# Optimization experiments

Hardware: AMD Instinct MI355X
Metric: run time of the kernel (lower is better)

## Reference

```python
import math
import jax, jax.numpy as jnp
import numpy as np

N_HEAD = 16

def new_gelu(x):
    # 0.5*x*(1+tanh(sqrt(2/pi)*(x+0.044715*x^3)))
    c = math.sqrt(2.0 / math.pi)
    return 0.5 * x * (1.0 + jnp.tanh(c * (x + 0.044715 * x * x * x)))

def setup_inputs() -> dict:
    key = jax.random.key(0)
    ks = jax.random.split(key, 9)
    B, T, C = 2, 2048, 1024
    s = lambda k, shape, fan: jax.random.normal(k, shape, dtype=jnp.float32) * (1.0 / math.sqrt(fan))
    return {
        "x": jax.random.normal(ks[0], (B, T, C), dtype=jnp.float32),
        "Wqkv": s(ks[1], (C, 3 * C), C),
        "bqkv": jnp.zeros((3 * C,), dtype=jnp.float32),
        "Wo": s(ks[2], (C, C), C),
        "bo": jnp.zeros((C,), dtype=jnp.float32),
        "Wfc": s(ks[3], (C, 4 * C), C),
        "bfc": jnp.zeros((4 * C,), dtype=jnp.float32),
        "Wproj": s(ks[4], (4 * C, C), 4 * C),
        "bproj": jnp.zeros((C,), dtype=jnp.float32),
    }

def attention(x, Wqkv, bqkv, Wo, bo):
    B, T, C = x.shape
    hd = C // N_HEAD
    xp = x @ Wqkv + bqkv                     # [B,T,3C]
    q, k, v = xp[:, :, :C], xp[:, :, C:2 * C], xp[:, :, 2 * C:]
    # Faithful to source: direct reshape [B,T,C] -> [B,nh,T,hd] (no transpose)
    q = q.reshape(B, N_HEAD, T, hd)
    k = k.reshape(B, N_HEAD, T, hd)
    v = v.reshape(B, N_HEAD, T, hd)
    att = jnp.einsum('bhqd,bhkd->bhqk', q, k) * (1.0 / math.sqrt(hd))
    causal = jnp.tril(jnp.ones((T, T), dtype=bool))
    att = jnp.where(causal, att, -jnp.inf)
    att = jax.nn.softmax(att, axis=-1)
    y = jnp.einsum('bhqk,bhkd->bhqd', att, v)  # [B,nh,T,hd]
    y = jnp.transpose(y, (0, 2, 1, 3)).reshape(B, T, C)
    return y @ Wo + bo

def reference(x, Wqkv, bqkv, Wo, bo, Wfc, bfc, Wproj, bproj):
    # Block.forward with layernorm=False (default), dropout in eval mode
    x = x + attention(x, Wqkv, bqkv, Wo, bo)
    mlpx = new_gelu(x @ Wfc + bfc) @ Wproj + bproj
    return x + mlpx
```

## Files before the change

### kernel.cpp

```cpp
#include <hip/hip_runtime.h>


typedef __attribute__((ext_vector_type(8))) short  bf16x8;
typedef __attribute__((ext_vector_type(4))) float  f32x4;
typedef __attribute__((ext_vector_type(8))) unsigned short u16x8;

__device__ __forceinline__ unsigned short bfu(float f) {
    union { float f; unsigned int u; } c; c.f = f;
    unsigned int u = c.u;
    unsigned int r = (u + 0x7fffu + ((u >> 16) & 1u)) >> 16;
    return (unsigned short)r;
}

__device__ __forceinline__ void gload_lds16(const void* g, void* l) {
    __builtin_amdgcn_global_load_lds(
        (const __attribute__((address_space(1))) void*)g,
        (__attribute__((address_space(3))) void*)l, 16, 0, 0);
}

__global__ __launch_bounds__(256) void cvt_bf16(const float* __restrict__ in,
                                                unsigned short* __restrict__ out) {
    size_t i = (size_t)blockIdx.x * 256 + threadIdx.x;
    const float4* p = (const float4*)in;
    float4 a = p[2 * i], b = p[2 * i + 1];
    u16x8 v;
    v[0] = bfu(a.x); v[1] = bfu(a.y); v[2] = bfu(a.z); v[3] = bfu(a.w);
    v[4] = bfu(b.x); v[5] = bfu(b.y); v[6] = bfu(b.z); v[7] = bfu(b.w);
    *(u16x8*)(out + 8 * i) = v;
}

__global__ __launch_bounds__(256) void wtrans(const float* __restrict__ W,
                                              unsigned short* __restrict__ Wt,
                                              int K, int N) {
    __shared__ float tile[32][33];
    int n0 = blockIdx.x * 32, k0 = blockIdx.y * 32;
    int tx = threadIdx.x & 31, ty = threadIdx.x >> 5;
#pragma unroll
    for (int r = 0; r < 32; r += 8)
        tile[ty + r][tx] = W[(size_t)(k0 + ty + r) * N + n0 + tx];
    __syncthreads();
#pragma unroll
    for (int r = 0; r < 32; r += 8)
        Wt[(size_t)(n0 + ty + r) * K + k0 + tx] = bfu(tile[tx][ty + r]);
}

template <int EPI>
__global__ __launch_bounds__(256) void gemm_bf16(
    const unsigned short* __restrict__ A, const unsigned short* __restrict__ Bt,
    const float* __restrict__ bias, const float* __restrict__ res,
    unsigned short* __restrict__ outb, float* __restrict__ outf,
    int M, int N, int K) {
    __shared__ __align__(16) unsigned short As[128 * 32];
    __shared__ __align__(16) unsigned short Bs[128 * 32];
    const int t = threadIdx.x;
    const int l = t & 63, w = t >> 6;
    const int lr = l & 15, lg = l >> 4;
    const int brow = blockIdx.y * 128, bcol = blockIdx.x * 128;
    const int wr = (w >> 1) * 64, wc = (w & 1) * 64;

    f32x4 acc[4][4];
#pragma unroll
    for (int m = 0; m < 4; ++m)
#pragma unroll
        for (int n = 0; n < 4; ++n) acc[m][n] = (f32x4){0.f, 0.f, 0.f, 0.f};

    const int ar = t >> 2, ac = (t & 3) * 8;
    const size_t Abase = (size_t)(brow + ar) * K + ac;
    const size_t Bbase = (size_t)(bcol + ar) * K + ac;
    char* la = (char*)As + w * 1024;
    char* lb = (char*)Bs + w * 1024;

    for (int kt = 0; kt < K; kt += 32) {
        gload_lds16(A + Abase + kt, la);
        gload_lds16(A + Abase + (size_t)64 * K + kt, la + 4096);
        gload_lds16(Bt + Bbase + kt, lb);
        gload_lds16(Bt + Bbase + (size_t)64 * K + kt, lb + 4096);
        __syncthreads();

        bf16x8 af[4], bfr[4];
#pragma unroll
        for (int m = 0; m < 4; ++m)
            af[m] = *(const bf16x8*)(As + (wr + m * 16 + lr) * 32 + lg * 8);
#pragma unroll
        for (int n = 0; n < 4; ++n)
            bfr[n] = *(const bf16x8*)(Bs + (wc + n * 16 + lr) * 32 + lg * 8);
#pragma unroll
        for (int m = 0; m < 4; ++m)
#pragma unroll
            for (int n = 0; n < 4; ++n)
                acc[m][n] = __builtin_amdgcn_mfma_f32_16x16x32_bf16(
                    af[m], bfr[n], acc[m][n], 0, 0, 0);
        __syncthreads();
    }

    float bv[4];
#pragma unroll
    for (int n = 0; n < 4; ++n) bv[n] = bias[bcol + wc + n * 16 + lr];
#pragma unroll
    for (int m = 0; m < 4; ++m) {
#pragma unroll
        for (int r = 0; r < 4; ++r) {
            const int row = brow + wr + m * 16 + lg * 4 + r;
#pragma unroll
            for (int n = 0; n < 4; ++n) {
                const int col = bcol + wc + n * 16 + lr;
                const size_t idx = (size_t)row * N + col;
                float v = acc[m][n][r] + bv[n];
                if constexpr (EPI == 0) {
                    outb[idx] = bfu(v);
                } else if constexpr (EPI == 1) {
                    v += res[idx];
                    outf[idx] = v;
                    outb[idx] = bfu(v);
                } else if constexpr (EPI == 2) {
                    float a = 0.7978845608f * (v + 0.044715f * v * v * v);
                    float g = v / (1.0f + __expf(-2.0f * a));
                    outb[idx] = bfu(g);
                } else {
                    v += res[idx];
                    outf[idx] = v;
                }
            }
        }
    }
}

__global__ __launch_bounds__(128) void attn(const unsigned short* __restrict__ xp,
                                            unsigned short* __restrict__ y) {
    __shared__ __align__(16) unsigned short Vt[64 * 72];
    __shared__ __align__(16) unsigned short Pl[2][32 * 72];
    const int t = threadIdx.x;
    const int l = t & 63, w = t >> 6;
    const int lr = l & 15, lg = l >> 4;
    const int bh = blockIdx.x >> 5;
    const int u = blockIdx.x & 31;
    const int qt = (u & 1) ? (31 - (u >> 1)) : (u >> 1);
    const int b = bh >> 4, h = bh & 15;
    const size_t hb = ((size_t)b * 2048 + h * 128) * 3072;
    const size_t rowb = (size_t)b * 2048;
    const int q0 = qt * 64 + w * 32;

    bf16x8 qf[2][2];
#pragma unroll
    for (int mq = 0; mq < 2; ++mq)
#pragma unroll
        for (int kk = 0; kk < 2; ++kk)
            qf[mq][kk] = *(const bf16x8*)(xp + hb + (size_t)((q0 >> 4) + mq) * 3072 +
                                          lr * 64 + kk * 32 + lg * 8);

    f32x4 o[2][4];
    float mx[2][4], ls[2][4];
#pragma unroll
    for (int mq = 0; mq < 2; ++mq)
#pragma unroll
        for (int n = 0; n < 4; ++n) o[mq][n] = (f32x4){0.f, 0.f, 0.f, 0.f};
#pragma unroll
    for (int mq = 0; mq < 2; ++mq)
#pragma unroll
        for (int r = 0; r < 4; ++r) { mx[mq][r] = -1e30f; ls[mq][r] = 0.f; }

    const int qmaxw = q0 + 31;
    const int ntiles = qt + 1;
    const int m32 = t & 31;
    const int cc = t >> 5;
    const float SC = 0.18033688f;

    for (int j = 0; j < ntiles; ++j) {
        const int kv0 = j * 64;
        __syncthreads();
#pragma unroll
        for (int it = 0; it < 4; ++it) {
            const int c = cc + it * 4;
            unsigned int xv[4];
#pragma unroll
            for (int n = 0; n < 4; ++n)
                xv[n] = *(const unsigned int*)(xp + hb + 2048 +
                                               (size_t)((kv0 >> 4) + n) * 3072 +
                                               c * 64 + 2 * m32);
            unsigned int lo0 = (xv[0] & 0xffffu) | (xv[1] << 16);
            unsigned int lo1 = (xv[2] & 0xffffu) | (xv[3] << 16);
            unsigned int hi0 = (xv[0] >> 16) | (xv[1] & 0xffff0000u);
            unsigned int hi1 = (xv[2] >> 16) | (xv[3] & 0xffff0000u);
            *(uint2*)(Vt + (2 * m32) * 72 + c * 4) = make_uint2(lo0, lo1);
            *(uint2*)(Vt + (2 * m32 + 1) * 72 + c * 4) = make_uint2(hi0, hi1);
        }
        __syncthreads();

        {
            f32x4 s[2][4];
#pragma unroll
            for (int mq = 0; mq < 2; ++mq)
#pragma unroll
                for (int n = 0; n < 4; ++n) s[mq][n] = (f32x4){0.f, 0.f, 0.f, 0.f};
#pragma unroll
            for (int kk = 0; kk < 2; ++kk)
#pragma unroll
                for (int n = 0; n < 4; ++n) {
                    bf16x8 kf = *(const bf16x8*)(xp + hb + 1024 +
                                                 (size_t)((kv0 >> 4) + n) * 3072 +
                                                 lr * 64 + kk * 32 + lg * 8);
#pragma unroll
                    for (int mq = 0; mq < 2; ++mq)
                        s[mq][n] = __builtin_amdgcn_mfma_f32_16x16x32_bf16(
                            qf[mq][kk], kf, s[mq][n], 0, 0, 0);
                }
            const bool needMask = (kv0 + 63) > q0;
#pragma unroll
            for (int mq = 0; mq < 2; ++mq)
#pragma unroll
                for (int n = 0; n < 4; ++n) {
                    s[mq][n] = s[mq][n] * SC;
                    if (needMask) {
                        const int col = kv0 + n * 16 + lr;
#pragma unroll
                        for (int r = 0; r < 4; ++r) {
                            const int row = q0 + mq * 16 + lg * 4 + r;
                            if (col > row) s[mq][n][r] = -1e30f;
                        }
                    }
                }
            float rmx[2][4], corr[2][4], rsum[2][4];
#pragma unroll
            for (int mq = 0; mq < 2; ++mq)
#pragma unroll
                for (int r = 0; r < 4; ++r)
                    rmx[mq][r] = fmaxf(fmaxf(s[mq][0][r], s[mq][1][r]),
                                       fmaxf(s[mq][2][r], s[mq][3][r]));
#pragma unroll
            for (int d = 1; d < 16; d <<= 1)
#pragma unroll
                for (int mq = 0; mq < 2; ++mq)
#pragma unroll
                    for (int r = 0; r < 4; ++r)
                        rmx[mq][r] = fmaxf(rmx[mq][r], __shfl_xor(rmx[mq][r], d, 64));
#pragma unroll
            for (int mq = 0; mq < 2; ++mq)
#pragma unroll
                for (int r = 0; r < 4; ++r) {
                    float mn = fmaxf(mx[mq][r], rmx[mq][r]);
                    corr[mq][r] = exp2f(mx[mq][r] - mn);
                    mx[mq][r] = mn;
                }
#pragma unroll
            for (int mq = 0; mq < 2; ++mq)
#pragma unroll
                for (int n = 0; n < 4; ++n)
#pragma unroll
                    for (int r = 0; r < 4; ++r)
                        s[mq][n][r] = exp2f(s[mq][n][r] - mx[mq][r]);
#pragma unroll
            for (int mq = 0; mq < 2; ++mq)
#pragma unroll
                for (int r = 0; r < 4; ++r)
                    rsum[mq][r] = s[mq][0][r] + s[mq][1][r] + s[mq][2][r] + s[mq][3][r];
#pragma unroll
            for (int d = 1; d < 16; d <<= 1)
#pragma unroll
                for (int mq = 0; mq < 2; ++mq)
#pragma unroll
                    for (int r = 0; r < 4; ++r)
                        rsum[mq][r] += __shfl_xor(rsum[mq][r], d, 64);
#pragma unroll
            for (int mq = 0; mq < 2; ++mq)
#pragma unroll
                for (int r = 0; r < 4; ++r)
                    ls[mq][r] = ls[mq][r] * corr[mq][r] + rsum[mq][r];
#pragma unroll
            for (int mq = 0; mq < 2; ++mq)
#pragma unroll
                for (int nd = 0; nd < 4; ++nd)
#pragma unroll
                    for (int r = 0; r < 4; ++r) o[mq][nd][r] *= corr[mq][r];
#pragma unroll
            for (int mq = 0; mq < 2; ++mq)
#pragma unroll
                for (int r = 0; r < 4; ++r) {
                    const int row = mq * 16 + lg * 4 + r;
                    unsigned int u0 = (unsigned)bfu(s[mq][0][r]) |
                                      ((unsigned)bfu(s[mq][1][r]) << 16);
                    unsigned int u1 = (unsigned)bfu(s[mq][2][r]) |
                                      ((unsigned)bfu(s[mq][3][r]) << 16);
                    *(uint2*)(&Pl[w][row * 72 + lr * 4]) = make_uint2(u0, u1);
                }
            asm volatile("s_waitcnt lgkmcnt(0)" ::: "memory");
            __builtin_amdgcn_sched_barrier(0);
#pragma unroll
            for (int kk = 0; kk < 2; ++kk) {
                bf16x8 pa[2];
                pa[0] = *(const bf16x8*)(&Pl[w][(lr) * 72 + kk * 32 + lg * 8]);
                pa[1] = *(const bf16x8*)(&Pl[w][(16 + lr) * 72 + kk * 32 + lg * 8]);
#pragma unroll
                for (int nd = 0; nd < 4; ++nd) {
                    bf16x8 vb = *(const bf16x8*)(Vt + (nd * 16 + lr) * 72 + kk * 32 + lg * 8);
                    o[0][nd] = __builtin_amdgcn_mfma_f32_16x16x32_bf16(pa[0], vb, o[0][nd], 0, 0, 0);
                    o[1][nd] = __builtin_amdgcn_mfma_f32_16x16x32_bf16(pa[1], vb, o[1][nd], 0, 0, 0);
                }
            }
        }
    }
#pragma unroll
    for (int mq = 0; mq < 2; ++mq)
#pragma unroll
        for (int r = 0; r < 4; ++r) {
            const float inv = 1.0f / ls[mq][r];
            const size_t row = rowb + q0 + mq * 16 + lg * 4 + r;
#pragma unroll
            for (int nd = 0; nd < 4; ++nd)
                y[row * 1024 + h * 64 + nd * 16 + lr] = bfu(o[mq][nd][r] * inv);
        }
}

extern "C" void kernel_launch(void* const* d_in, const int* in_sizes, int n_in,
                              void* d_out, int out_size, void* d_ws, size_t ws_size,
                              hipStream_t stream) {
    const float* x     = (const float*)d_in[0];
    const float* Wqkv  = (const float*)d_in[1];
    const float* bqkv  = (const float*)d_in[2];
    const float* Wo    = (const float*)d_in[3];
    const float* bo    = (const float*)d_in[4];
    const float* Wfc   = (const float*)d_in[5];
    const float* bfc   = (const float*)d_in[6];
    const float* Wproj = (const float*)d_in[7];
    const float* bproj = (const float*)d_in[8];
    float* out = (float*)d_out;

    char* p = (char*)d_ws;
    unsigned short* xb     = (unsigned short*)(p);
    unsigned short* xpb    = (unsigned short*)(p + (8ull << 20));
    unsigned short* hbuf   = (unsigned short*)(p);
    unsigned short* ybuf   = (unsigned short*)(p + (32ull << 20));
    float*          x1     = (float*)(p + (40ull << 20));
    unsigned short* x1b    = (unsigned short*)(p + (56ull << 20));
    unsigned short* WqkvT  = (unsigned short*)(p + (64ull << 20));
    unsigned short* WoT    = (unsigned short*)(p + (70ull << 20));
    unsigned short* WfcT   = (unsigned short*)(p + (72ull << 20));
    unsigned short* WprojT = (unsigned short*)(p + (80ull << 20));

    cvt_bf16<<<dim3(2048), 256, 0, stream>>>(x, xb);
    wtrans<<<dim3(96, 32), 256, 0, stream>>>(Wqkv, WqkvT, 1024, 3072);
    wtrans<<<dim3(32, 32), 256, 0, stream>>>(Wo, WoT, 1024, 1024);
    wtrans<<<dim3(128, 32), 256, 0, stream>>>(Wfc, WfcT, 1024, 4096);
    wtrans<<<dim3(32, 128), 256, 0, stream>>>(Wproj, WprojT, 4096, 1024);

    gemm_bf16<0><<<dim3(24, 32), 256, 0, stream>>>(xb, WqkvT, bqkv, nullptr,
                                                   xpb, nullptr, 4096, 3072, 1024);
    attn<<<dim3(1024), 128, 0, stream>>>(xpb, ybuf);
    gemm_bf16<1><<<dim3(8, 32), 256, 0, stream>>>(ybuf, WoT, bo, x,
                                                  x1b, x1, 4096, 1024, 1024);
    gemm_bf16<2><<<dim3(32, 32), 256, 0, stream>>>(x1b, WfcT, bfc, nullptr,
                                                   hbuf, nullptr, 4096, 4096, 1024);
    gemm_bf16<3><<<dim3(8, 32), 256, 0, stream>>>(hbuf, WprojT, bproj, x1,
                                                  nullptr, out, 4096, 1024, 4096);
}
```

Baseline: 487.5 us.

## Split attention KV loop across four wave groups with LDS softmax merge

The attention kernel now runs 512 threads per block: four groups of two waves each take every fourth KV tile for the same 64-query tile. The groups' partial output, max and sum states are then combined through shared memory with a two-step log-sum-exp merge. Block order is also changed so the longest query tiles launch first instead of interleaving short and long tiles. This targets long serial KV loops on the late query tiles and poor load balance. In exchange it adds extra block-wide barriers, 72KB of LDS per block and merge overhead, and the 4-wide KV split leaves groups idle on short tiles.

Result: faster. 460.1 us (-5.6%).

```diff
diff --git a/kernel.cpp b/kernel.cpp
--- a/kernel.cpp
+++ b/kernel.cpp
@@ -125,27 +125,30 @@
     }
 }
 
-__global__ __launch_bounds__(128) void attn(const unsigned short* __restrict__ xp,
-                                            unsigned short* __restrict__ y) {
-    __shared__ __align__(16) unsigned short Vt[64 * 72];
-    __shared__ __align__(16) unsigned short Pl[2][32 * 72];
+__global__ __launch_bounds__(512, 4) void attn(const unsigned short* __restrict__ xp,
+                                               unsigned short* __restrict__ y) {
+    __shared__ __align__(16) char smem[73728];
     const int t = threadIdx.x;
     const int l = t & 63, w = t >> 6;
+    const int s = w & 1, g = w >> 1;
     const int lr = l & 15, lg = l >> 4;
-    const int bh = blockIdx.x >> 5;
-    const int u = blockIdx.x & 31;
-    const int qt = (u & 1) ? (31 - (u >> 1)) : (u >> 1);
+    const int qt = 31 - (blockIdx.x >> 5);
+    const int bh = blockIdx.x & 31;
     const int b = bh >> 4, h = bh & 15;
     const size_t hb = ((size_t)b * 2048 + h * 128) * 3072;
     const size_t rowb = (size_t)b * 2048;
-    const int q0 = qt * 64 + w * 32;
+    const int q0 = qt * 64;
+    const int qmin = q0 + s * 32;
+
+    unsigned short* Vtg = (unsigned short*)smem + g * (64 * 72);
+    unsigned short* Plw = (unsigned short*)(smem + 36864) + w * (32 * 72);
 
     bf16x8 qf[2][2];
 #pragma unroll
     for (int mq = 0; mq < 2; ++mq)
 #pragma unroll
         for (int kk = 0; kk < 2; ++kk)
-            qf[mq][kk] = *(const bf16x8*)(xp + hb + (size_t)((q0 >> 4) + mq) * 3072 +
+            qf[mq][kk] = *(const bf16x8*)(xp + hb + (size_t)((qmin >> 4) + mq) * 3072 +
                                           lr * 64 + kk * 32 + lg * 8);
 
     f32x4 o[2][4];
@@ -159,39 +162,44 @@
 #pragma unroll
         for (int r = 0; r < 4; ++r) { mx[mq][r] = -1e30f; ls[mq][r] = 0.f; }
 
-    const int qmaxw = q0 + 31;
     const int ntiles = qt + 1;
-    const int m32 = t & 31;
-    const int cc = t >> 5;
+    const int niter = (qt + 4) >> 2;
+    const int tg = s * 64 + l;
+    const int m32 = tg & 31;
+    const int cc = tg >> 5;
     const float SC = 0.18033688f;
 
-    for (int j = 0; j < ntiles; ++j) {
+    for (int jj = 0; jj < niter; ++jj) {
+        const int j = jj * 4 + g;
+        const bool active = (j < ntiles);
         const int kv0 = j * 64;
         __syncthreads();
-#pragma unroll
-        for (int it = 0; it < 4; ++it) {
-            const int c = cc + it * 4;
-            unsigned int xv[4];
-#pragma unroll
-            for (int n = 0; n < 4; ++n)
-                xv[n] = *(const unsigned int*)(xp + hb + 2048 +
-                                               (size_t)((kv0 >> 4) + n) * 3072 +
-                                               c * 64 + 2 * m32);
-            unsigned int lo0 = (xv[0] & 0xffffu) | (xv[1] << 16);
-            unsigned int lo1 = (xv[2] & 0xffffu) | (xv[3] << 16);
-            unsigned int hi0 = (xv[0] >> 16) | (xv[1] & 0xffff0000u);
-            unsigned int hi1 = (xv[2] >> 16) | (xv[3] & 0xffff0000u);
-            *(uint2*)(Vt + (2 * m32) * 72 + c * 4) = make_uint2(lo0, lo1);
-            *(uint2*)(Vt + (2 * m32 + 1) * 72 + c * 4) = make_uint2(hi0, hi1);
+        if (active) {
+#pragma unroll
+            for (int it = 0; it < 4; ++it) {
+                const int c = cc + it * 4;
+                unsigned int xv[4];
+#pragma unroll
+                for (int n = 0; n < 4; ++n)
+                    xv[n] = *(const unsigned int*)(xp + hb + 2048 +
+                                                   (size_t)((kv0 >> 4) + n) * 3072 +
+                                                   c * 64 + 2 * m32);
+                unsigned int lo0 = (xv[0] & 0xffffu) | (xv[1] << 16);
+                unsigned int lo1 = (xv[2] & 0xffffu) | (xv[3] << 16);
+                unsigned int hi0 = (xv[0] >> 16) | (xv[1] & 0xffff0000u);
+                unsigned int hi1 = (xv[2] >> 16) | (xv[3] & 0xffff0000u);
+                *(uint2*)(Vtg + (2 * m32) * 72 + c * 4) = make_uint2(lo0, lo1);
+                *(uint2*)(Vtg + (2 * m32 + 1) * 72 + c * 4) = make_uint2(hi0, hi1);
+            }
         }
         __syncthreads();
 
-        {
-            f32x4 s[2][4];
-#pragma unroll
-            for (int mq = 0; mq < 2; ++mq)
-#pragma unroll
-                for (int n = 0; n < 4; ++n) s[mq][n] = (f32x4){0.f, 0.f, 0.f, 0.f};
+        if (active) {
+            f32x4 sv[2][4];
+#pragma unroll
+            for (int mq = 0; mq < 2; ++mq)
+#pragma unroll
+                for (int n = 0; n < 4; ++n) sv[mq][n] = (f32x4){0.f, 0.f, 0.f, 0.f};
 #pragma unroll
             for (int kk = 0; kk < 2; ++kk)
 #pragma unroll
@@ -201,21 +209,21 @@
                                                  lr * 64 + kk * 32 + lg * 8);
 #pragma unroll
                     for (int mq = 0; mq < 2; ++mq)
-                        s[mq][n] = __builtin_amdgcn_mfma_f32_16x16x32_bf16(
-                            qf[mq][kk], kf, s[mq][n], 0, 0, 0);
-                }
-            const bool needMask = (kv0 + 63) > q0;
+                        sv[mq][n] = __builtin_amdgcn_mfma_f32_16x16x32_bf16(
+                            qf[mq][kk], kf, sv[mq][n], 0, 0, 0);
+                }
+            const bool needMask = (kv0 + 63) > qmin;
 #pragma unroll
             for (int mq = 0; mq < 2; ++mq)
 #pragma unroll
                 for (int n = 0; n < 4; ++n) {
-                    s[mq][n] = s[mq][n] * SC;
+                    sv[mq][n] = sv[mq][n] * SC;
                     if (needMask) {
                         const int col = kv0 + n * 16 + lr;
 #pragma unroll
                         for (int r = 0; r < 4; ++r) {
-                            const int row = q0 + mq * 16 + lg * 4 + r;
-                            if (col > row) s[mq][n][r] = -1e30f;
+                            const int row = qmin + mq * 16 + lg * 4 + r;
+                            if (col > row) sv[mq][n][r] = -1e30f;
                         }
                     }
                 }
@@ -224,8 +232,8 @@
             for (int mq = 0; mq < 2; ++mq)
 #pragma unroll
                 for (int r = 0; r < 4; ++r)
-                    rmx[mq][r] = fmaxf(fmaxf(s[mq][0][r], s[mq][1][r]),
-                                       fmaxf(s[mq][2][r], s[mq][3][r]));
+                    rmx[mq][r] = fmaxf(fmaxf(sv[mq][0][r], sv[mq][1][r]),
+                                       fmaxf(sv[mq][2][r], sv[mq][3][r]));
 #pragma unroll
             for (int d = 1; d < 16; d <<= 1)
 #pragma unroll
@@ -247,12 +255,12 @@
                 for (int n = 0; n < 4; ++n)
 #pragma unroll
                     for (int r = 0; r < 4; ++r)
-                        s[mq][n][r] = exp2f(s[mq][n][r] - mx[mq][r]);
+                        sv[mq][n][r] = exp2f(sv[mq][n][r] - mx[mq][r]);
 #pragma unroll
             for (int mq = 0; mq < 2; ++mq)
 #pragma unroll
                 for (int r = 0; r < 4; ++r)
-                    rsum[mq][r] = s[mq][0][r] + s[mq][1][r] + s[mq][2][r] + s[mq][3][r];
+                    rsum[mq][r] = sv[mq][0][r] + sv[mq][1][r] + sv[mq][2][r] + sv[mq][3][r];
 #pragma unroll
             for (int d = 1; d < 16; d <<= 1)
 #pragma unroll
@@ -276,38 +284,86 @@
 #pragma unroll
                 for (int r = 0; r < 4; ++r) {
                     const int row = mq * 16 + lg * 4 + r;
-                    unsigned int u0 = (unsigned)bfu(s[mq][0][r]) |
-                                      ((unsigned)bfu(s[mq][1][r]) << 16);
-                    unsigned int u1 = (unsigned)bfu(s[mq][2][r]) |
-                                      ((unsigned)bfu(s[mq][3][r]) << 16);
-                    *(uint2*)(&Pl[w][row * 72 + lr * 4]) = make_uint2(u0, u1);
+                    unsigned int u0 = (unsigned)bfu(sv[mq][0][r]) |
+                                      ((unsigned)bfu(sv[mq][1][r]) << 16);
+                    unsigned int u1 = (unsigned)bfu(sv[mq][2][r]) |
+                                      ((unsigned)bfu(sv[mq][3][r]) << 16);
+                    *(uint2*)(Plw + row * 72 + lr * 4) = make_uint2(u0, u1);
                 }
             asm volatile("s_waitcnt lgkmcnt(0)" ::: "memory");
             __builtin_amdgcn_sched_barrier(0);
 #pragma unroll
             for (int kk = 0; kk < 2; ++kk) {
                 bf16x8 pa[2];
-                pa[0] = *(const bf16x8*)(&Pl[w][(lr) * 72 + kk * 32 + lg * 8]);
-                pa[1] = *(const bf16x8*)(&Pl[w][(16 + lr) * 72 + kk * 32 + lg * 8]);
+                pa[0] = *(const bf16x8*)(Plw + (lr) * 72 + kk * 32 + lg * 8);
+                pa[1] = *(const bf16x8*)(Plw + (16 + lr) * 72 + kk * 32 + lg * 8);
 #pragma unroll
                 for (int nd = 0; nd < 4; ++nd) {
-                    bf16x8 vb = *(const bf16x8*)(Vt + (nd * 16 + lr) * 72 + kk * 32 + lg * 8);
+                    bf16x8 vb = *(const bf16x8*)(Vtg + (nd * 16 + lr) * 72 + kk * 32 + lg * 8);
                     o[0][nd] = __builtin_amdgcn_mfma_f32_16x16x32_bf16(pa[0], vb, o[0][nd], 0, 0, 0);
                     o[1][nd] = __builtin_amdgcn_mfma_f32_16x16x32_bf16(pa[1], vb, o[1][nd], 0, 0, 0);
                 }
             }
         }
     }
-#pragma unroll
-    for (int mq = 0; mq < 2; ++mq)
-#pragma unroll
-        for (int r = 0; r < 4; ++r) {
-            const float inv = 1.0f / ls[mq][r];
-            const size_t row = rowb + q0 + mq * 16 + lg * 4 + r;
+
+    float* buf = (float*)smem;
+    auto bufw = [&](int bi) {
+        float* q = buf + (size_t)(bi * 64 + l) * 52;
+#pragma unroll
+        for (int mq = 0; mq < 2; ++mq) {
 #pragma unroll
             for (int nd = 0; nd < 4; ++nd)
-                y[row * 1024 + h * 64 + nd * 16 + lr] = bfu(o[mq][nd][r] * inv);
+                *(f32x4*)(q + mq * 16 + nd * 4) = o[mq][nd];
+            f32x4 mv = {mx[mq][0], mx[mq][1], mx[mq][2], mx[mq][3]};
+            f32x4 lv = {ls[mq][0], ls[mq][1], ls[mq][2], ls[mq][3]};
+            *(f32x4*)(q + 32 + mq * 4) = mv;
+            *(f32x4*)(q + 40 + mq * 4) = lv;
         }
+    };
+    auto bufm = [&](int bi) {
+        const float* q = buf + (size_t)(bi * 64 + l) * 52;
+#pragma unroll
+        for (int mq = 0; mq < 2; ++mq) {
+            f32x4 mv = *(const f32x4*)(q + 32 + mq * 4);
+            f32x4 lv = *(const f32x4*)(q + 40 + mq * 4);
+            f32x4 ob[4];
+#pragma unroll
+            for (int nd = 0; nd < 4; ++nd)
+                ob[nd] = *(const f32x4*)(q + mq * 16 + nd * 4);
+#pragma unroll
+            for (int r = 0; r < 4; ++r) {
+                float mn = fmaxf(mx[mq][r], mv[r]);
+                float ca = exp2f(mx[mq][r] - mn);
+                float cb = exp2f(mv[r] - mn);
+                mx[mq][r] = mn;
+                ls[mq][r] = ls[mq][r] * ca + lv[r] * cb;
+#pragma unroll
+                for (int nd = 0; nd < 4; ++nd)
+                    o[mq][nd][r] = o[mq][nd][r] * ca + ob[nd][r] * cb;
+            }
+        }
+    };
+    __syncthreads();
+    if (g >= 2) bufw(s * 2 + (g - 2));
+    __syncthreads();
+    if (g < 2) bufm(s * 2 + g);
+    __syncthreads();
+    if (g == 1) bufw(s * 2);
+    __syncthreads();
+    if (g == 0) {
+        bufm(s * 2);
+#pragma unroll
+        for (int mq = 0; mq < 2; ++mq)
+#pragma unroll
+            for (int r = 0; r < 4; ++r) {
+                const float inv = 1.0f / ls[mq][r];
+                const size_t row = rowb + qmin + mq * 16 + lg * 4 + r;
+#pragma unroll
+                for (int nd = 0; nd < 4; ++nd)
+                    y[row * 1024 + h * 64 + nd * 16 + lr] = bfu(o[mq][nd][r] * inv);
+            }
+    }
 }
 
 extern "C" void kernel_launch(void* const* d_in, const int* in_sizes, int n_in,
@@ -344,7 +400,7 @@
 
     gemm_bf16<0><<<dim3(24, 32), 256, 0, stream>>>(xb, WqkvT, bqkv, nullptr,
                                                    xpb, nullptr, 4096, 3072, 1024);
-    attn<<<dim3(1024), 128, 0, stream>>>(xpb, ybuf);
+    attn<<<dim3(1024), 512, 0, stream>>>(xpb, ybuf);
     gemm_bf16<1><<<dim3(8, 32), 256, 0, stream>>>(ybuf, WoT, bo, x,
                                                   x1b, x1, 4096, 1024, 1024);
     gemm_bf16<2><<<dim3(32, 32), 256, 0, stream>>>(x1b, WfcT, bfc, nullptr,
```
